# Kernel optimization log

Measured on AMD Instinct MI355X. Metric: run time of the kernel, lower is better.

Reference implementation:

```python
import jax, jax.numpy as jnp
import numpy as np

D = 128      # embedding_dim
E = 50000    # positive edges per metapath
S = 16       # negative samples per edge
N_A = 100000 # nodes of type A (head type of both metapaths)
N_B = 50000  # nodes of type B (tail type of metapath 1)


def setup_inputs() -> dict:
    key = jax.random.key(0)
    ks = jax.random.split(key, 10)
    emb_A = jax.random.normal(ks[0], (N_A, D), dtype=jnp.float32)
    emb_B = jax.random.normal(ks[1], (N_B, D), dtype=jnp.float32)
    # nn.init.uniform_(a=-1, b=1)
    rel_emb = jax.random.uniform(ks[2], (2, D, D), dtype=jnp.float32, minval=-1.0, maxval=1.0)
    edge_index_m0 = jax.random.randint(ks[3], (2, E), 0, N_A)  # A -> A
    edge_index_m1 = jnp.stack([
        jax.random.randint(ks[4], (E,), 0, N_A),               # heads: type A
        jax.random.randint(ks[5], (E,), 0, N_B),               # tails: type B
    ])
    neg_head_m0 = jax.random.randint(ks[6], (E, S), 0, N_A)
    neg_head_m1 = jax.random.randint(ks[7], (E, S), 0, N_A)
    neg_tail_m0 = jax.random.randint(ks[8], (E, S), 0, N_A)
    neg_tail_m1 = jax.random.randint(ks[9], (E, S), 0, N_B)
    return dict(emb_A=emb_A, emb_B=emb_B, rel_emb=rel_emb,
                edge_index_m0=edge_index_m0, edge_index_m1=edge_index_m1,
                neg_head_m0=neg_head_m0, neg_head_m1=neg_head_m1,
                neg_tail_m0=neg_tail_m0, neg_tail_m1=neg_tail_m1)


# The torch module computes score = (A K B^T).sum(dim=1); summing the [E,E]
# score matrix over dim 1 equals contracting with sum_j b_j, so we never
# materialize the [E,E] (or [E*S, E*S]) matrix -- same math, fused reduction.

def _pos_score(K, emb_h, emb_t, edge_index):
    s = emb_t[edge_index[1]].sum(0)          # [d] = sum_j b_j
    return emb_h[edge_index[0]] @ (K @ s)    # [E]


def _neg_head_score(K, emb_h, neg):
    # predict(mode='head'): emb_A = emb_h[neg.reshape(-1)],
    # idx_B = edge_index[0][arange(E)*S] == neg[:, 0],
    # side_B = (K @ emb_h[idx_B].T).repeat_interleave(S, -1); sum over columns
    # == K @ (S * sum_j emb_h[neg[j, 0]]).
    s = neg.shape[1]
    c = K @ (s * emb_h[neg[:, 0]].sum(0))    # [d]
    return emb_h[neg.reshape(-1)] @ c        # [E*S]


def _neg_tail_score(K, emb_t, neg):
    # predict(mode='tail'): emb_B = emb_t[neg.reshape(-1)],
    # idx_A = edge_index[1][arange(E)*S] == neg[:, 0],
    # side_A = (emb_t[idx_A] @ K).repeat_interleave(S, 0); row sums of
    # side_A @ emb_B^T == side_A @ sum_j emb_B[j].
    s = neg.shape[1]
    sb = emb_t[neg.reshape(-1)].sum(0)       # [d]
    base = (emb_t[neg[:, 0]] @ K) @ sb       # [E]
    return jnp.repeat(base, s)               # [E*S]


def reference(emb_A, emb_B, rel_emb, edge_index_m0, edge_index_m1,
              neg_head_m0, neg_head_m1, neg_tail_m0, neg_tail_m1):
    K0, K1 = rel_emb[0], rel_emb[1]
    pos0 = _pos_score(K0, emb_A, emb_A, edge_index_m0)   # [E]
    pos1 = _pos_score(K1, emb_A, emb_B, edge_index_m1)   # [E]
    nh0 = _neg_head_score(K0, emb_A, neg_head_m0)        # [E*S]
    nh1 = _neg_head_score(K1, emb_A, neg_head_m1)        # [E*S]
    nt0 = _neg_tail_score(K0, emb_A, neg_tail_m0)        # [E*S]
    nt1 = _neg_tail_score(K1, emb_B, neg_tail_m1)        # [E*S]
    return jnp.concatenate([pos0, pos1, nh0, nh1, nt0, nt1])
```

## Files before the change

kernel.cpp:

```cpp
#include <hip/hip_runtime.h>
#include <stdint.h>

#define D 128
#define E_EDGES 50000
#define S_NEG 16
#define N_A 100000
#define N_B 50000
#define ES (E_EDGES * S_NEG)

#define HW 12500
#define ACH 38
#define BCH 34

#define GA1 500
#define GB1 250
#define RPG 25
#define RA2 20
#define RB2 10
#define GA2 391
#define GB2 196

__device__ inline float dot4(float4 a, float4 b) {
    return a.x * b.x + a.y * b.y + a.z * b.z + a.w * b.w;
}
__device__ inline void fma16(float* acc, const float4 w, const float4 x) {
    acc[0]  += w.x * x.x; acc[1]  += w.x * x.y; acc[2]  += w.x * x.z; acc[3]  += w.x * x.w;
    acc[4]  += w.y * x.x; acc[5]  += w.y * x.y; acc[6]  += w.y * x.z; acc[7]  += w.y * x.w;
    acc[8]  += w.z * x.x; acc[9]  += w.z * x.y; acc[10] += w.z * x.z; acc[11] += w.z * x.w;
    acc[12] += w.w * x.x; acc[13] += w.w * x.y; acc[14] += w.w * x.z; acc[15] += w.w * x.w;
}
__device__ inline void fma8(float* acc, const float2 w, const float4 x) {
    acc[0] += w.x * x.x; acc[1] += w.x * x.y; acc[2] += w.x * x.z; acc[3] += w.x * x.w;
    acc[4] += w.y * x.x; acc[5] += w.y * x.y; acc[6] += w.y * x.z; acc[7] += w.y * x.w;
}


__global__ void k_hist(const int* __restrict__ ei0, const int* __restrict__ ei1,
                       const int* __restrict__ nh0, const int* __restrict__ nh1,
                       const int* __restrict__ nt0, const int* __restrict__ nt1,
                       uint32_t* __restrict__ partA, uint32_t* __restrict__ partB) {
    __shared__ uint32_t h[HW];
    const int tid = threadIdx.x;
    for (int w = tid; w < HW; w += 512) h[w] = 0;
    __syncthreads();

    const int b = blockIdx.x;
    if (b < 2 * ACH) {
        const int c = b >> 1, hh = b & 1;
        const unsigned lo = hh * 50000u;
        uint32_t* dst = partA + (size_t)b * HW;
        if (c >= 2 && c < 6) {
            const int* src = (c < 4) ? nh0 : nh1;
            const long long base = (long long)(c & 1) * 25000 * S_NEG;
            for (int i = tid; i < 25000; i += 512) {
                const unsigned r = (unsigned)src[base + (long long)i * S_NEG] - lo;
                if (r < 50000u) atomicAdd(&h[r >> 2], 1u << ((r & 3u) * 8u));
            }
        } else {
            const int* srcp = (c < 2) ? (ei0 + E_EDGES + c * 25000)
                                      : (nt0 + (c - 6) * 25000);
            const int4* src4 = reinterpret_cast<const int4*>(srcp);
            for (int i = tid; i < 6250; i += 512) {
                const int4 v = src4[i];
                unsigned r;
                r = (unsigned)v.x - lo; if (r < 50000u) atomicAdd(&h[r >> 2], 1u << ((r & 3u) * 8u));
                r = (unsigned)v.y - lo; if (r < 50000u) atomicAdd(&h[r >> 2], 1u << ((r & 3u) * 8u));
                r = (unsigned)v.z - lo; if (r < 50000u) atomicAdd(&h[r >> 2], 1u << ((r & 3u) * 8u));
                r = (unsigned)v.w - lo; if (r < 50000u) atomicAdd(&h[r >> 2], 1u << ((r & 3u) * 8u));
            }
        }
        __syncthreads();
        for (int w = tid; w < HW; w += 512) dst[w] = h[w];
    } else {
        const int c = b - 2 * ACH;
        uint32_t* dst = partB + (size_t)c * HW;
        const int* srcp = (c < 2) ? (ei1 + E_EDGES + c * 25000)
                                  : (nt1 + (c - 2) * 25000);
        const int4* src4 = reinterpret_cast<const int4*>(srcp);
        for (int i = tid; i < 6250; i += 512) {
            const int4 v = src4[i];
            unsigned r;
            r = (unsigned)v.x; if (r < 50000u) atomicAdd(&h[r >> 2], 1u << ((r & 3u) * 8u));
            r = (unsigned)v.y; if (r < 50000u) atomicAdd(&h[r >> 2], 1u << ((r & 3u) * 8u));
            r = (unsigned)v.z; if (r < 50000u) atomicAdd(&h[r >> 2], 1u << ((r & 3u) * 8u));
            r = (unsigned)v.w; if (r < 50000u) atomicAdd(&h[r >> 2], 1u << ((r & 3u) * 8u));
        }
        __syncthreads();
        for (int w = tid; w < HW; w += 512) dst[w] = h[w];
    }
}

__global__ void k_reduceC(const uint32_t* __restrict__ partA,
                          const uint32_t* __restrict__ partB,
                          float4* __restrict__ cwA, float2* __restrict__ cwB) {
    const int t = blockIdx.x * 256 + threadIdx.x;
    if (t < N_A) {
        const int n = t;
        const int hh = (n >= 50000);
        const int w = (n - hh * 50000) >> 2;
        const int sh = (n & 3) * 8;
        const uint32_t* p = partA + (size_t)hh * HW + w;
        unsigned s0 = 0, s1 = 0, s2 = 0, s3 = 0;
#pragma unroll
        for (int c = 0; c < 2; ++c)  s0 += (p[(size_t)(c * 2) * HW] >> sh) & 255u;
#pragma unroll
        for (int c = 2; c < 4; ++c)  s1 += (p[(size_t)(c * 2) * HW] >> sh) & 255u;
#pragma unroll
        for (int c = 4; c < 6; ++c)  s2 += (p[(size_t)(c * 2) * HW] >> sh) & 255u;
#pragma unroll 8
        for (int c = 6; c < 38; ++c) s3 += (p[(size_t)(c * 2) * HW] >> sh) & 255u;
        cwA[n] = make_float4((float)s0, (float)s1, (float)s2, (float)s3);
    } else if (t < N_A + N_B) {
        const int n = t - N_A;
        const int w = n >> 2;
        const int sh = (n & 3) * 8;
        const uint32_t* p = partB + w;
        unsigned s0 = 0, s1 = 0;
#pragma unroll
        for (int c = 0; c < 2; ++c)  s0 += (p[(size_t)c * HW] >> sh) & 255u;
#pragma unroll 8
        for (int c = 2; c < 34; ++c) s1 += (p[(size_t)c * HW] >> sh) & 255u;
        cwB[n] = make_float2((float)s0, (float)s1);
    }
}

__global__ void __launch_bounds__(256, 4)
k_scan1(const float* __restrict__ embA, const float* __restrict__ embB,
        const float4* __restrict__ cwA, const float2* __restrict__ cwB,
        float* __restrict__ psumA, float* __restrict__ psumB) {
    __shared__ float sds[4 * 512];
    const int tid = threadIdx.x;
    const int l = tid & 31;
    const int grp = tid >> 5;
    const int wid = tid >> 6;

    if ((int)blockIdx.x < GA1) {
        const int r0 = (blockIdx.x * 8 + grp) * RPG;
        const float* base = embA + 4 * l;
        float acc[16];
#pragma unroll
        for (int k = 0; k < 16; ++k) acc[k] = 0.f;
        float4 wc[5], xc[5];
#pragma unroll
        for (int u = 0; u < 5; ++u) {
            wc[u] = cwA[r0 + u];
            xc[u] = *reinterpret_cast<const float4*>(base + (size_t)(r0 + u) * D);
        }
#pragma unroll
        for (int b = 0; b < 5; ++b) {
            float4 wn[5], xn[5];
            if (b < 4) {
#pragma unroll
                for (int u = 0; u < 5; ++u) {
                    const int rr = r0 + (b + 1) * 5 + u;
                    wn[u] = cwA[rr];
                    xn[u] = *reinterpret_cast<const float4*>(base + (size_t)rr * D);
                }
            }
#pragma unroll
            for (int u = 0; u < 5; ++u) fma16(acc, wc[u], xc[u]);
            if (b < 4) {
#pragma unroll
                for (int u = 0; u < 5; ++u) { wc[u] = wn[u]; xc[u] = xn[u]; }
            }
        }
#pragma unroll
        for (int k = 0; k < 16; ++k) acc[k] += __shfl_xor(acc[k], 32);
        if ((tid & 32) == 0) {
            float* w0 = sds + wid * 512;
#pragma unroll
            for (int p = 0; p < 4; ++p)
                *reinterpret_cast<float4*>(w0 + p * 128 + 4 * l) =
                    make_float4(acc[4 * p], acc[4 * p + 1], acc[4 * p + 2], acc[4 * p + 3]);
        }
        __syncthreads();
        for (int j = tid; j < 512; j += 256)
            psumA[(size_t)blockIdx.x * 512 + j] =
                sds[j] + sds[512 + j] + sds[1024 + j] + sds[1536 + j];
    } else {
        const int r0 = ((blockIdx.x - GA1) * 8 + grp) * RPG;
        const float* base = embB + 4 * l;
        float acc[8];
#pragma unroll
        for (int k = 0; k < 8; ++k) acc[k] = 0.f;
        float2 wc[5]; float4 xc[5];
#pragma unroll
        for (int u = 0; u < 5; ++u) {
            wc[u] = cwB[r0 + u];
            xc[u] = *reinterpret_cast<const float4*>(base + (size_t)(r0 + u) * D);
        }
#pragma unroll
        for (int b = 0; b < 5; ++b) {
            float2 wn[5]; float4 xn[5];
            if (b < 4) {
#pragma unroll
                for (int u = 0; u < 5; ++u) {
                    const int rr = r0 + (b + 1) * 5 + u;
                    wn[u] = cwB[rr];
                    xn[u] = *reinterpret_cast<const float4*>(base + (size_t)rr * D);
                }
            }
#pragma unroll
            for (int u = 0; u < 5; ++u) fma8(acc, wc[u], xc[u]);
            if (b < 4) {
#pragma unroll
                for (int u = 0; u < 5; ++u) { wc[u] = wn[u]; xc[u] = xn[u]; }
            }
        }
#pragma unroll
        for (int k = 0; k < 8; ++k) acc[k] += __shfl_xor(acc[k], 32);
        if ((tid & 32) == 0) {
            float* w0 = sds + wid * 256;
#pragma unroll
            for (int p = 0; p < 2; ++p)
                *reinterpret_cast<float4*>(w0 + p * 128 + 4 * l) =
                    make_float4(acc[4 * p], acc[4 * p + 1], acc[4 * p + 2], acc[4 * p + 3]);
        }
        __syncthreads();
        for (int j = tid; j < 256; j += 256)
            psumB[(size_t)(blockIdx.x - GA1) * 256 + j] =
                sds[j] + sds[256 + j] + sds[512 + j] + sds[768 + j];
    }
}

__global__ void k_red1(const float* __restrict__ psumA, const float* __restrict__ psumB,
                       float* __restrict__ psumA2, float* __restrict__ psumB2) {
    const int b = blockIdx.x, t = threadIdx.x;
    if (b < RA2) {
        const float* p = psumA + (size_t)b * 25 * 512;
        float s0 = 0.f, s1 = 0.f;
#pragma unroll 5
        for (int r = 0; r < 25; ++r) { s0 += p[r * 512 + t]; s1 += p[r * 512 + 256 + t]; }
        psumA2[(size_t)b * 512 + t] = s0;
        psumA2[(size_t)b * 512 + 256 + t] = s1;
    } else {
        const int bi = b - RA2;
        const float* p = psumB + (size_t)bi * 25 * 256;
        float s = 0.f;
#pragma unroll 5
        for (int r = 0; r < 25; ++r) s += p[r * 256 + t];
        psumB2[(size_t)bi * 256 + t] = s;
    }
}

__global__ void k_cvec2(const float* __restrict__ rel,
                        const float* __restrict__ psumA2, const float* __restrict__ psumB2,
                        float* __restrict__ cvec) {
    const int j = blockIdx.x;
    const int tid = threadIdx.x;
    __shared__ float Kds[D * 129];
    __shared__ float red[256];
    __shared__ float sv[D];
    const float* Kp = rel + (size_t)(j & 1) * D * D;

    for (int e = tid; e < D * D / 4; e += 256) {
        const int row = e >> 5, col = (e & 31) * 4;
        const float4 v = *reinterpret_cast<const float4*>(Kp + (size_t)row * D + col);
        float* dst = Kds + row * 129 + col;
        dst[0] = v.x; dst[1] = v.y; dst[2] = v.z; dst[3] = v.w;
    }

    const int g = tid >> 7, i = tid & 127;
    float s = 0.f;
    if (j == 1 || j == 5) {
        const int plane = (j == 1) ? 0 : 1;
        for (int b = g; b < RB2; b += 2) s += psumB2[(size_t)b * 256 + plane * D + i];
    } else {
        const int plane = (j == 0) ? 0 : (j - 1);
        for (int b = g; b < RA2; b += 2) s += psumA2[(size_t)b * 512 + plane * D + i];
    }
    red[tid] = s;
    __syncthreads();
    if (tid < 128) sv[i] = red[i] + red[128 + i];
    __syncthreads();

    if (tid < 128) {
        const float scale = (j == 2 || j == 3) ? (float)S_NEG : 1.0f;
        float acc = 0.f;
#pragma unroll
        for (int k = 0; k < D; k += 4)
            acc += Kds[i * 129 + k] * sv[k] + Kds[i * 129 + k + 1] * sv[k + 1]
                 + Kds[i * 129 + k + 2] * sv[k + 2] + Kds[i * 129 + k + 3] * sv[k + 3];
        cvec[j * D + i] = acc * scale;
    }
}

__global__ void __launch_bounds__(256, 4)
k_scan2(const float* __restrict__ embA, const float* __restrict__ embB,
        const float* __restrict__ cvec, float* __restrict__ PA,
        float* __restrict__ PB) {
    __shared__ float sc[5 * D];
    const int tid = threadIdx.x;

    if ((int)blockIdx.x < GA2) {
        for (int j = tid; j < 5 * D; j += 256) sc[j] = cvec[j];
        __syncthreads();
        const int n = blockIdx.x * 256 + tid;
        const int nc = min(n, N_A - 1);
        const float4* row = reinterpret_cast<const float4*>(embA + (size_t)nc * D);
        float a0 = 0.f, a1 = 0.f, a2 = 0.f, a3 = 0.f, a4 = 0.f;
#pragma unroll 8
        for (int k = 0; k < 32; ++k) {
            const float4 x = row[k];
            a0 += dot4(x, *reinterpret_cast<const float4*>(sc + 0 * D + 4 * k));
            a1 += dot4(x, *reinterpret_cast<const float4*>(sc + 1 * D + 4 * k));
            a2 += dot4(x, *reinterpret_cast<const float4*>(sc + 2 * D + 4 * k));
            a3 += dot4(x, *reinterpret_cast<const float4*>(sc + 3 * D + 4 * k));
            a4 += dot4(x, *reinterpret_cast<const float4*>(sc + 4 * D + 4 * k));
        }
        if (n < N_A) {
            PA[0 * (size_t)N_A + n] = a0;
            PA[1 * (size_t)N_A + n] = a1;
            PA[2 * (size_t)N_A + n] = a2;
            PA[3 * (size_t)N_A + n] = a3;
            PA[4 * (size_t)N_A + n] = a4;
        }
    } else {
        for (int j = tid; j < D; j += 256) sc[j] = cvec[5 * D + j];
        __syncthreads();
        const int n = (blockIdx.x - GA2) * 256 + tid;
        const int nc = min(n, N_B - 1);
        const float4* row = reinterpret_cast<const float4*>(embB + (size_t)nc * D);
        float a0 = 0.f;
#pragma unroll 8
        for (int k = 0; k < 32; ++k) {
            const float4 x = row[k];
            a0 += dot4(x, *reinterpret_cast<const float4*>(sc + 4 * k));
        }
        if (n < N_B) PB[n] = a0;
    }
}

__global__ void k_scatter(const int* __restrict__ ei0, const int* __restrict__ ei1,
                          const int* __restrict__ nh0, const int* __restrict__ nh1,
                          const int* __restrict__ nt0, const int* __restrict__ nt1,
                          const float* __restrict__ PA, const float* __restrict__ PB,
                          float* __restrict__ out) {
    const int total4 = (2 * E_EDGES + 4 * ES) / 4;
    const float* P0 = PA;
    const float* P1 = PA + (size_t)N_A;
    const float* P2 = PA + (size_t)2 * N_A;
    const float* P3 = PA + (size_t)3 * N_A;
    const float* P4 = PA + (size_t)4 * N_A;
    for (int t = blockIdx.x * blockDim.x + threadIdx.x; t < total4;
         t += gridDim.x * blockDim.x) {
        const int e = t * 4;
        float4 v;
        if (e < E_EDGES) {
            const int4 i4 = *reinterpret_cast<const int4*>(ei0 + e);
            v = make_float4(P0[i4.x], P0[i4.y], P0[i4.z], P0[i4.w]);
        } else if (e < 2 * E_EDGES) {
            const int4 i4 = *reinterpret_cast<const int4*>(ei1 + (e - E_EDGES));
            v = make_float4(P1[i4.x], P1[i4.y], P1[i4.z], P1[i4.w]);
        } else if (e < 2 * E_EDGES + ES) {
            const int4 i4 = *reinterpret_cast<const int4*>(nh0 + (e - 2 * E_EDGES));
            v = make_float4(P2[i4.x], P2[i4.y], P2[i4.z], P2[i4.w]);
        } else if (e < 2 * E_EDGES + 2 * ES) {
            const int4 i4 = *reinterpret_cast<const int4*>(nh1 + (e - 2 * E_EDGES - ES));
            v = make_float4(P3[i4.x], P3[i4.y], P3[i4.z], P3[i4.w]);
        } else if (e < 2 * E_EDGES + 3 * ES) {
            const int i = e - 2 * E_EDGES - 2 * ES;
            const float s = P4[nt0[(i >> 4) << 4]];
            v = make_float4(s, s, s, s);
        } else {
            const int i = e - 2 * E_EDGES - 3 * ES;
            const float s = PB[nt1[(i >> 4) << 4]];
            v = make_float4(s, s, s, s);
        }
        *reinterpret_cast<float4*>(out + e) = v;
    }
}

extern "C" void kernel_launch(void* const* d_in, const int* in_sizes, int n_in,
                              void* d_out, int out_size, void* d_ws, size_t ws_size,
                              hipStream_t stream) {
    const float* embA = (const float*)d_in[0];
    const float* embB = (const float*)d_in[1];
    const float* rel  = (const float*)d_in[2];
    const int* ei0 = (const int*)d_in[3];
    const int* ei1 = (const int*)d_in[4];
    const int* nh0 = (const int*)d_in[5];
    const int* nh1 = (const int*)d_in[6];
    const int* nt0 = (const int*)d_in[7];
    const int* nt1 = (const int*)d_in[8];
    float* out = (float*)d_out;

    uint32_t* partA = (uint32_t*)d_ws;
    uint32_t* partB = partA + (size_t)2 * ACH * HW;
    float4* cwA = (float4*)(partB + (size_t)BCH * HW);
    float2* cwB = (float2*)(cwA + N_A);
    float* psumA = (float*)(cwB + N_B);
    float* psumB = psumA + (size_t)GA1 * 512;
    float* psumA2 = psumB + (size_t)GB1 * 256;
    float* psumB2 = psumA2 + (size_t)RA2 * 512;
    float* cvec  = psumB2 + (size_t)RB2 * 256;
    float* PA    = cvec + 6 * D;
    float* PB    = PA + (size_t)5 * N_A;

    k_hist<<<2 * ACH + BCH, 512, 0, stream>>>(ei0, ei1, nh0, nh1, nt0, nt1, partA, partB);
    k_reduceC<<<(N_A + N_B + 255) / 256, 256, 0, stream>>>(partA, partB, cwA, cwB);
    k_scan1<<<GA1 + GB1, 256, 0, stream>>>(embA, embB, cwA, cwB, psumA, psumB);
    k_red1<<<RA2 + RB2, 256, 0, stream>>>(psumA, psumB, psumA2, psumB2);
    k_cvec2<<<6, 256, 0, stream>>>(rel, psumA2, psumB2, cvec);
    k_scan2<<<GA2 + GB2, 256, 0, stream>>>(embA, embB, cvec, PA, PB);
    k_scatter<<<2048, 256, 0, stream>>>(ei0, ei1, nh0, nh1, nt0, nt1, PA, PB, out);
}
```

Before: 192.2 us.

## Fuse histogram reduction, partial-sum reduction and K·s into scan kernels

The per-node histogram count reduction moves into k_scan1, which stores the counts in shared memory. Block partial sums are accumulated with atomics into 16 replicated copies of the sum vectors, and every k_scan2 block redundantly computes the K·s projection. Together these remove three kernel launches (k_reduceC, k_red1, k_cvec2) and their intermediate global buffers. In exchange, each scan2 block re-reads the 6x128x128 relation matrices and reduces the 16 copies, and float atomics make the summation order nondeterministic.

```diff
diff --git a/kernel.cpp b/kernel.cpp
--- a/kernel.cpp
+++ b/kernel.cpp
@@ -14,9 +14,7 @@
 
 #define GA1 500
 #define GB1 250
-#define RPG 25
-#define RA2 20
-#define RB2 10
+#define NCPY 16
 #define GA2 391
 #define GB2 196
 
@@ -38,9 +36,13 @@
 __global__ void k_hist(const int* __restrict__ ei0, const int* __restrict__ ei1,
                        const int* __restrict__ nh0, const int* __restrict__ nh1,
                        const int* __restrict__ nt0, const int* __restrict__ nt1,
-                       uint32_t* __restrict__ partA, uint32_t* __restrict__ partB) {
+                       uint32_t* __restrict__ partA, uint32_t* __restrict__ partB,
+                       float* __restrict__ svec) {
     __shared__ uint32_t h[HW];
     const int tid = threadIdx.x;
+    if (blockIdx.x == 0) {
+        for (int i = tid; i < NCPY * 6 * D; i += 512) svec[i] = 0.f;
+    }
     for (int w = tid; w < HW; w += 512) h[w] = 0;
     __syncthreads();
 
@@ -90,52 +92,40 @@
     }
 }
 
-__global__ void k_reduceC(const uint32_t* __restrict__ partA,
-                          const uint32_t* __restrict__ partB,
-                          float4* __restrict__ cwA, float2* __restrict__ cwB) {
-    const int t = blockIdx.x * 256 + threadIdx.x;
-    if (t < N_A) {
-        const int n = t;
-        const int hh = (n >= 50000);
-        const int w = (n - hh * 50000) >> 2;
-        const int sh = (n & 3) * 8;
-        const uint32_t* p = partA + (size_t)hh * HW + w;
-        unsigned s0 = 0, s1 = 0, s2 = 0, s3 = 0;
-#pragma unroll
-        for (int c = 0; c < 2; ++c)  s0 += (p[(size_t)(c * 2) * HW] >> sh) & 255u;
-#pragma unroll
-        for (int c = 2; c < 4; ++c)  s1 += (p[(size_t)(c * 2) * HW] >> sh) & 255u;
-#pragma unroll
-        for (int c = 4; c < 6; ++c)  s2 += (p[(size_t)(c * 2) * HW] >> sh) & 255u;
-#pragma unroll 8
-        for (int c = 6; c < 38; ++c) s3 += (p[(size_t)(c * 2) * HW] >> sh) & 255u;
-        cwA[n] = make_float4((float)s0, (float)s1, (float)s2, (float)s3);
-    } else if (t < N_A + N_B) {
-        const int n = t - N_A;
-        const int w = n >> 2;
-        const int sh = (n & 3) * 8;
-        const uint32_t* p = partB + w;
-        unsigned s0 = 0, s1 = 0;
-#pragma unroll
-        for (int c = 0; c < 2; ++c)  s0 += (p[(size_t)c * HW] >> sh) & 255u;
-#pragma unroll 8
-        for (int c = 2; c < 34; ++c) s1 += (p[(size_t)c * HW] >> sh) & 255u;
-        cwB[n] = make_float2((float)s0, (float)s1);
-    }
-}
-
 __global__ void __launch_bounds__(256, 4)
 k_scan1(const float* __restrict__ embA, const float* __restrict__ embB,
-        const float4* __restrict__ cwA, const float2* __restrict__ cwB,
-        float* __restrict__ psumA, float* __restrict__ psumB) {
+        const uint32_t* __restrict__ partA, const uint32_t* __restrict__ partB,
+        float* __restrict__ svec) {
     __shared__ float sds[4 * 512];
+    __shared__ float4 cwbuf[200];
     const int tid = threadIdx.x;
     const int l = tid & 31;
     const int grp = tid >> 5;
     const int wid = tid >> 6;
+    float* svdst = svec + (size_t)(blockIdx.x & (NCPY - 1)) * (6 * D);
 
     if ((int)blockIdx.x < GA1) {
-        const int r0 = (blockIdx.x * 8 + grp) * RPG;
+        const int nb = blockIdx.x * 200;
+        if (tid < 200) {
+            const int n = nb + tid;
+            const int hh = (n >= 50000);
+            const int sh = (n & 3) * 8;
+            const uint32_t* p = partA + (size_t)hh * HW + ((n - hh * 50000) >> 2);
+            unsigned s0 = 0, s1 = 0, s2 = 0, s3 = 0;
+#pragma unroll
+            for (int c = 0; c < 2; ++c)  s0 += (p[(size_t)(c * 2) * HW] >> sh) & 255u;
+#pragma unroll
+            for (int c = 2; c < 4; ++c)  s1 += (p[(size_t)(c * 2) * HW] >> sh) & 255u;
+#pragma unroll
+            for (int c = 4; c < 6; ++c)  s2 += (p[(size_t)(c * 2) * HW] >> sh) & 255u;
+#pragma unroll 8
+            for (int c = 6; c < 38; ++c) s3 += (p[(size_t)(c * 2) * HW] >> sh) & 255u;
+            cwbuf[tid] = make_float4((float)s0, (float)s1, (float)s2, (float)s3);
+        }
+        __syncthreads();
+
+        const int r0 = nb + grp * 25;
+        const int lr0 = grp * 25;
         const float* base = embA + 4 * l;
         float acc[16];
 #pragma unroll
@@ -143,7 +133,7 @@
         float4 wc[5], xc[5];
 #pragma unroll
         for (int u = 0; u < 5; ++u) {
-            wc[u] = cwA[r0 + u];
+            wc[u] = cwbuf[lr0 + u];
             xc[u] = *reinterpret_cast<const float4*>(base + (size_t)(r0 + u) * D);
         }
 #pragma unroll
@@ -152,9 +142,9 @@
             if (b < 4) {
 #pragma unroll
                 for (int u = 0; u < 5; ++u) {
-                    const int rr = r0 + (b + 1) * 5 + u;
-                    wn[u] = cwA[rr];
-                    xn[u] = *reinterpret_cast<const float4*>(base + (size_t)rr * D);
+                    const int rr = (b + 1) * 5 + u;
+                    wn[u] = cwbuf[lr0 + rr];
+                    xn[u] = *reinterpret_cast<const float4*>(base + (size_t)(r0 + rr) * D);
                 }
             }
 #pragma unroll
@@ -175,10 +165,25 @@
         }
         __syncthreads();
         for (int j = tid; j < 512; j += 256)
-            psumA[(size_t)blockIdx.x * 512 + j] =
-                sds[j] + sds[512 + j] + sds[1024 + j] + sds[1536 + j];
+            atomicAdd(&svdst[j], sds[j] + sds[512 + j] + sds[1024 + j] + sds[1536 + j]);
     } else {
-        const int r0 = ((blockIdx.x - GA1) * 8 + grp) * RPG;
+        const int nb = (blockIdx.x - GA1) * 200;
+        if (tid < 200) {
+            const int n = nb + tid;
+            const int sh = (n & 3) * 8;
+            const uint32_t* p = partB + (n >> 2);
+            unsigned s0 = 0, s1 = 0;
+#pragma unroll
+            for (int c = 0; c < 2; ++c)  s0 += (p[(size_t)c * HW] >> sh) & 255u;
+#pragma unroll 8
+            for (int c = 2; c < 34; ++c) s1 += (p[(size_t)c * HW] >> sh) & 255u;
+            reinterpret_cast<float2*>(cwbuf)[tid] = make_float2((float)s0, (float)s1);
+        }
+        __syncthreads();
+        const float2* cw2 = reinterpret_cast<const float2*>(cwbuf);
+
+        const int r0 = nb + grp * 25;
+        const int lr0 = grp * 25;
         const float* base = embB + 4 * l;
         float acc[8];
 #pragma unroll
@@ -186,7 +191,7 @@
         float2 wc[5]; float4 xc[5];
 #pragma unroll
         for (int u = 0; u < 5; ++u) {
-            wc[u] = cwB[r0 + u];
+            wc[u] = cw2[lr0 + u];
             xc[u] = *reinterpret_cast<const float4*>(base + (size_t)(r0 + u) * D);
         }
 #pragma unroll
@@ -195,9 +200,9 @@
             if (b < 4) {
 #pragma unroll
                 for (int u = 0; u < 5; ++u) {
-                    const int rr = r0 + (b + 1) * 5 + u;
-                    wn[u] = cwB[rr];
-                    xn[u] = *reinterpret_cast<const float4*>(base + (size_t)rr * D);
+                    const int rr = (b + 1) * 5 + u;
+                    wn[u] = cw2[lr0 + rr];
+                    xn[u] = *reinterpret_cast<const float4*>(base + (size_t)(r0 + rr) * D);
                 }
             }
 #pragma unroll
@@ -218,83 +223,44 @@
         }
         __syncthreads();
         for (int j = tid; j < 256; j += 256)
-            psumB[(size_t)(blockIdx.x - GA1) * 256 + j] =
-                sds[j] + sds[256 + j] + sds[512 + j] + sds[768 + j];
-    }
-}
-
-__global__ void k_red1(const float* __restrict__ psumA, const float* __restrict__ psumB,
-                       float* __restrict__ psumA2, float* __restrict__ psumB2) {
-    const int b = blockIdx.x, t = threadIdx.x;
-    if (b < RA2) {
-        const float* p = psumA + (size_t)b * 25 * 512;
-        float s0 = 0.f, s1 = 0.f;
-#pragma unroll 5
-        for (int r = 0; r < 25; ++r) { s0 += p[r * 512 + t]; s1 += p[r * 512 + 256 + t]; }
-        psumA2[(size_t)b * 512 + t] = s0;
-        psumA2[(size_t)b * 512 + 256 + t] = s1;
-    } else {
-        const int bi = b - RA2;
-        const float* p = psumB + (size_t)bi * 25 * 256;
-        float s = 0.f;
-#pragma unroll 5
-        for (int r = 0; r < 25; ++r) s += p[r * 256 + t];
-        psumB2[(size_t)bi * 256 + t] = s;
-    }
-}
-
-__global__ void k_cvec2(const float* __restrict__ rel,
-                        const float* __restrict__ psumA2, const float* __restrict__ psumB2,
-                        float* __restrict__ cvec) {
-    const int j = blockIdx.x;
-    const int tid = threadIdx.x;
-    __shared__ float Kds[D * 129];
-    __shared__ float red[256];
-    __shared__ float sv[D];
-    const float* Kp = rel + (size_t)(j & 1) * D * D;
-
-    for (int e = tid; e < D * D / 4; e += 256) {
-        const int row = e >> 5, col = (e & 31) * 4;
-        const float4 v = *reinterpret_cast<const float4*>(Kp + (size_t)row * D + col);
-        float* dst = Kds + row * 129 + col;
-        dst[0] = v.x; dst[1] = v.y; dst[2] = v.z; dst[3] = v.w;
-    }
-
-    const int g = tid >> 7, i = tid & 127;
-    float s = 0.f;
-    if (j == 1 || j == 5) {
-        const int plane = (j == 1) ? 0 : 1;
-        for (int b = g; b < RB2; b += 2) s += psumB2[(size_t)b * 256 + plane * D + i];
-    } else {
-        const int plane = (j == 0) ? 0 : (j - 1);
-        for (int b = g; b < RA2; b += 2) s += psumA2[(size_t)b * 512 + plane * D + i];
-    }
-    red[tid] = s;
-    __syncthreads();
-    if (tid < 128) sv[i] = red[i] + red[128 + i];
-    __syncthreads();
-
-    if (tid < 128) {
-        const float scale = (j == 2 || j == 3) ? (float)S_NEG : 1.0f;
-        float acc = 0.f;
-#pragma unroll
-        for (int k = 0; k < D; k += 4)
-            acc += Kds[i * 129 + k] * sv[k] + Kds[i * 129 + k + 1] * sv[k + 1]
-                 + Kds[i * 129 + k + 2] * sv[k + 2] + Kds[i * 129 + k + 3] * sv[k + 3];
-        cvec[j * D + i] = acc * scale;
+            atomicAdd(&svdst[512 + j], sds[j] + sds[256 + j] + sds[512 + j] + sds[768 + j]);
     }
 }
 
 __global__ void __launch_bounds__(256, 4)
 k_scan2(const float* __restrict__ embA, const float* __restrict__ embB,
-        const float* __restrict__ cvec, float* __restrict__ PA,
-        float* __restrict__ PB) {
-    __shared__ float sc[5 * D];
+        const float* __restrict__ rel, const float* __restrict__ svec,
+        float* __restrict__ PA, float* __restrict__ PB) {
+    __shared__ float sv[6 * D];
+    __shared__ float sc[6 * D];
     const int tid = threadIdx.x;
 
+    for (int e = tid; e < 6 * D; e += 256) {
+        float s = 0.f;
+#pragma unroll
+        for (int c = 0; c < NCPY; ++c) s += svec[c * (6 * D) + e];
+        sv[e] = s;
+    }
+    __syncthreads();
+
+    for (int e = tid; e < 6 * D; e += 256) {
+        const int j = e >> 7, i = e & 127;
+        const int plane = (j == 0) ? 0 : (j == 1) ? 4 : (j == 5) ? 5 : (j - 1);
+        const float4* Kp4 = reinterpret_cast<const float4*>(
+            rel + (size_t)(j & 1) * (D * D) + (size_t)i * D);
+        const float* s = sv + plane * D;
+        float acc = 0.f;
+#pragma unroll
+        for (int k = 0; k < 32; ++k) {
+            const float4 kk = Kp4[k];
+            acc += kk.x * s[4 * k] + kk.y * s[4 * k + 1]
+                 + kk.z * s[4 * k + 2] + kk.w * s[4 * k + 3];
+        }
+        sc[e] = acc * ((j == 2 || j == 3) ? (float)S_NEG : 1.0f);
+    }
+    __syncthreads();
+
     if ((int)blockIdx.x < GA2) {
-        for (int j = tid; j < 5 * D; j += 256) sc[j] = cvec[j];
-        __syncthreads();
         const int n = blockIdx.x * 256 + tid;
         const int nc = min(n, N_A - 1);
         const float4* row = reinterpret_cast<const float4*>(embA + (size_t)nc * D);
@@ -316,8 +282,6 @@
             PA[4 * (size_t)N_A + n] = a4;
         }
     } else {
-        for (int j = tid; j < D; j += 256) sc[j] = cvec[5 * D + j];
-        __syncthreads();
         const int n = (blockIdx.x - GA2) * 256 + tid;
         const int nc = min(n, N_B - 1);
         const float4* row = reinterpret_cast<const float4*>(embB + (size_t)nc * D);
@@ -325,7 +289,7 @@
 #pragma unroll 8
         for (int k = 0; k < 32; ++k) {
             const float4 x = row[k];
-            a0 += dot4(x, *reinterpret_cast<const float4*>(sc + 4 * k));
+            a0 += dot4(x, *reinterpret_cast<const float4*>(sc + 5 * D + 4 * k));
         }
         if (n < N_B) PB[n] = a0;
     }
@@ -387,21 +351,13 @@
 
     uint32_t* partA = (uint32_t*)d_ws;
     uint32_t* partB = partA + (size_t)2 * ACH * HW;
-    float4* cwA = (float4*)(partB + (size_t)BCH * HW);
-    float2* cwB = (float2*)(cwA + N_A);
-    float* psumA = (float*)(cwB + N_B);
-    float* psumB = psumA + (size_t)GA1 * 512;
-    float* psumA2 = psumB + (size_t)GB1 * 256;
-    float* psumB2 = psumA2 + (size_t)RA2 * 512;
-    float* cvec  = psumB2 + (size_t)RB2 * 256;
-    float* PA    = cvec + 6 * D;
-    float* PB    = PA + (size_t)5 * N_A;
-
-    k_hist<<<2 * ACH + BCH, 512, 0, stream>>>(ei0, ei1, nh0, nh1, nt0, nt1, partA, partB);
-    k_reduceC<<<(N_A + N_B + 255) / 256, 256, 0, stream>>>(partA, partB, cwA, cwB);
-    k_scan1<<<GA1 + GB1, 256, 0, stream>>>(embA, embB, cwA, cwB, psumA, psumB);
-    k_red1<<<RA2 + RB2, 256, 0, stream>>>(psumA, psumB, psumA2, psumB2);
-    k_cvec2<<<6, 256, 0, stream>>>(rel, psumA2, psumB2, cvec);
-    k_scan2<<<GA2 + GB2, 256, 0, stream>>>(embA, embB, cvec, PA, PB);
+    float* svec = (float*)(partB + (size_t)BCH * HW);
+    float* PA   = svec + (size_t)NCPY * 6 * D;
+    float* PB   = PA + (size_t)5 * N_A;
+
+    k_hist<<<2 * ACH + BCH, 512, 0, stream>>>(ei0, ei1, nh0, nh1, nt0, nt1,
+                                              partA, partB, svec);
+    k_scan1<<<GA1 + GB1, 256, 0, stream>>>(embA, embB, partA, partB, svec);
+    k_scan2<<<GA2 + GB2, 256, 0, stream>>>(embA, embB, rel, svec, PA, PB);
     k_scatter<<<2048, 256, 0, stream>>>(ei0, ei1, nh0, nh1, nt0, nt1, PA, PB, out);
 }
```

Result: slower. 220.5 us (+14.7%).
